# Optimization experiments

Hardware: AMD Instinct MI355X
Metric: run time of the kernel (lower is better)

## Reference

```python
import jax, jax.numpy as jnp
import numpy as np

N = 4096          # n_neurons
M = 10            # max_memory
T = 10            # max_ticks
B = 1024          # batch
P = N // 2 // 2   # n_pairs = 1024
AD = 64           # attention_dim


def ln(x, g, b, eps=1e-5):
    m = x.mean(-1, keepdims=True)
    v = ((x - m) ** 2).mean(-1, keepdims=True)
    return (x - m) * jax.lax.rsqrt(v + eps) * g + b


def setup_inputs() -> dict:
    key = jax.random.key(0)
    ks = iter(jax.random.split(key, 64))

    def rn(shape, s=0.05):
        return (jax.random.normal(next(ks), shape) * s).astype(jnp.float32)

    d = {}
    d['x'] = jax.random.normal(next(ks), (B, 1, 28, 28), dtype=jnp.float32)
    d['post0'] = jax.random.normal(next(ks), (N, M), dtype=jnp.float32)
    d['pre0'] = jax.random.normal(next(ks), (N, M), dtype=jnp.float32)
    d['pairs'] = jax.random.randint(next(ks), (P, 2), 0, N)
    d['decay'] = jnp.full((P,), 0.1, jnp.float32)
    # image encoder: 784 -> 128 -> 32 -> 4
    d['ie_w1'] = rn((784, 128)); d['ie_b1'] = jnp.zeros(128); d['ie_g1'] = jnp.ones(128); d['ie_be1'] = jnp.zeros(128)
    d['ie_w2'] = rn((128, 32));  d['ie_b2'] = jnp.zeros(32);  d['ie_g2'] = jnp.ones(32);  d['ie_be2'] = jnp.zeros(32)
    d['ie_w3'] = rn((32, 4));    d['ie_b3'] = jnp.zeros(4)
    # synapse model: (4+N) -> 256 -> N
    d['sy_w1'] = rn((4 + N, 256)); d['sy_b1'] = jnp.zeros(256); d['sy_g'] = jnp.ones(256); d['sy_be'] = jnp.zeros(256)
    d['sy_w2'] = rn((256, N));     d['sy_b2'] = jnp.zeros(N)
    # batched per-neuron models: M -> 128 -> 1
    d['nm_w1'] = rn((N, M, 128)); d['nm_b1'] = jnp.zeros((N, 128))
    d['nm_g'] = jnp.ones((N, 128)); d['nm_be'] = jnp.zeros((N, 128))
    d['nm_w2'] = rn((N, 128));    d['nm_b2'] = jnp.zeros(N)
    # attention projections
    d['key_w'] = rn((4, AD)); d['key_b'] = jnp.zeros(AD)
    d['val_w'] = rn((4, AD)); d['val_b'] = jnp.zeros(AD)
    d['q_w'] = rn((P, AD));   d['q_b'] = jnp.zeros(AD)
    # syncronization reader: (AD+P) -> 512 -> 64 -> 10
    d['rd_w1'] = rn((AD + P, 512)); d['rd_b1'] = jnp.zeros(512); d['rd_g1'] = jnp.ones(512); d['rd_be1'] = jnp.zeros(512)
    d['rd_w2'] = rn((512, 64));     d['rd_b2'] = jnp.zeros(64);  d['rd_g2'] = jnp.ones(64);  d['rd_be2'] = jnp.zeros(64)
    d['rd_w3'] = rn((64, 10));      d['rd_b3'] = jnp.zeros(10)
    return d


def reference(x, post0, pre0, pairs, decay,
              ie_w1, ie_b1, ie_g1, ie_be1, ie_w2, ie_b2, ie_g2, ie_be2, ie_w3, ie_b3,
              sy_w1, sy_b1, sy_g, sy_be, sy_w2, sy_b2,
              nm_w1, nm_b1, nm_g, nm_be, nm_w2, nm_b2,
              key_w, key_b, val_w, val_b, q_w, q_b,
              rd_w1, rd_b1, rd_g1, rd_be1, rd_w2, rd_b2, rd_g2, rd_be2, rd_w3, rd_b3):
    b = x.shape[0]
    fx = x.reshape(b, -1)
    # image encoder
    e = jax.nn.relu(ln(fx @ ie_w1 + ie_b1, ie_g1, ie_be1))
    e = jax.nn.relu(ln(e @ ie_w2 + ie_b2, ie_g2, ie_be2))
    enc = e @ ie_w3 + ie_b3                               # [B,4]
    keys = enc @ key_w + key_b                            # [B,AD]
    values = enc @ val_w + val_b                          # [B,AD]
    post, pre = post0, pre0
    pred = None
    for tick in range(T):
        last_post = jnp.broadcast_to(post[:, -1][None, :], (b, N))
        syn_in = jnp.concatenate([enc, last_post], axis=1)            # [B,4+N]
        h = jax.nn.relu(ln(syn_in @ sy_w1 + sy_b1, sy_g, sy_be))
        new_pre = h @ sy_w2 + sy_b2                                   # [B,N]
        pre = jnp.concatenate([pre[:, 1:], new_pre.mean(0)[:, None]], axis=1)
        # batched per-neuron MLP over history
        h2 = jax.nn.relu(ln(jnp.einsum('nm,nmh->nh', pre, nm_w1) + nm_b1, nm_g, nm_be))
        new_post = jnp.einsum('nh,nh->n', h2, nm_w2) + nm_b2          # [N]
        post = jnp.concatenate([post[:, 1:], new_post[:, None]], axis=1)
        # decayed pair synchronization
        L = min(tick + 1, M)
        Zi = post[pairs[:, 0], M - L:]                                # [P,L]
        Zj = post[pairs[:, 1], M - L:]
        td = jnp.arange(L - 1, -1, -1, dtype=post.dtype)              # [L]
        R = jnp.exp(-decay[:, None] * td[None, :])                    # [P,L]
        sync = jnp.sum(Zi * R * Zj, axis=1) / (jnp.sum(R, axis=1) + 1e-8)  # [P]
        sv = jnp.broadcast_to(sync[None, :], (b, P))                  # [B,P]
        q = sv @ q_w + q_b                                            # [B,AD]
        scores = jnp.sum(q * keys, axis=-1, keepdims=True) / jnp.sqrt(jnp.float32(AD))
        aw = jax.nn.softmax(scores, axis=-1)                          # [B,1] -> ones
        att = aw * values                                             # [B,AD]
        comb = jnp.concatenate([att, sv], axis=-1)                    # [B,AD+P]
        r = jax.nn.relu(ln(comb @ rd_w1 + rd_b1, rd_g1, rd_be1))
        r = jax.nn.relu(ln(r @ rd_w2 + rd_b2, rd_g2, rd_be2))
        pred = r @ rd_w3 + rd_b3                                      # [B,10]
    return pred
```

## Files before the change

### kernel.cpp

```cpp
#include <hip/hip_runtime.h>

#define N_ 4096
#define M_ 10
#define T_ 10
#define B_ 1024
#define P_ 1024
#define NBLK 256
#define NTHR 512

__device__ __forceinline__ float wave_red_sum(float v) {
#pragma unroll
  for (int m = 32; m >= 1; m >>= 1) v += __shfl_xor(v, m);
  return v;
}

__device__ __forceinline__ float gld(const float* p) {
  return __hip_atomic_load(p, __ATOMIC_RELAXED, __HIP_MEMORY_SCOPE_AGENT);
}
__device__ __forceinline__ void gst(float* p, float v) {
  __hip_atomic_store(p, v, __ATOMIC_RELAXED, __HIP_MEMORY_SCOPE_AGENT);
}
__device__ __forceinline__ unsigned ld_u(unsigned* p) {
  return __hip_atomic_load(p, __ATOMIC_RELAXED, __HIP_MEMORY_SCOPE_AGENT);
}

__device__ __forceinline__ void drain_sync() {
  asm volatile("s_waitcnt vmcnt(0)" ::: "memory");
  __syncthreads();
}
__device__ __forceinline__ void arrive8(unsigned* line8, int g) {
  if (threadIdx.x == 0)
    __hip_atomic_fetch_add(&line8[(g & 7) * 32], 1u, __ATOMIC_RELAXED, __HIP_MEMORY_SCOPE_AGENT);
}
__device__ __forceinline__ void wait_sum8(unsigned* line8, unsigned target) {
  if (threadIdx.x == 0) {
    unsigned s;
    do {
      s = 0;
#pragma unroll
      for (int i = 0; i < 8; ++i) s += ld_u(&line8[i * 32]);
      if (s < target) __builtin_amdgcn_s_sleep(1);
    } while (s < target);
  }
  __syncthreads();
}
__device__ __forceinline__ void wait_word(unsigned* f, unsigned target) {
  if (threadIdx.x == 0) {
    while (ld_u(f) < target) __builtin_amdgcn_s_sleep(1);
  }
  __syncthreads();
}

__global__ void k_init(unsigned* __restrict__ bar) {
  if (threadIdx.x < 1024)
    __hip_atomic_store(bar + threadIdx.x, 0u, __ATOMIC_RELAXED, __HIP_MEMORY_SCOPE_AGENT);
}

struct MArgs {
  const float *x, *post0, *pre0;
  const int* pairs;
  const float* decay;
  const float *iew1, *ieb1, *ieg1, *iebe1, *iew2, *ieb2, *ieg2, *iebe2, *iew3, *ieb3;
  const float *syw1, *syb1, *syg, *sybe, *syw2, *syb2;
  const float *nw1, *nb1, *ng, *nbe, *nw2, *nb2;
  const float *vw, *vb;
  const float *rdw1, *rdb1, *rdg1, *rdbe1, *rdw2, *rdb2, *rdg2, *rdbe2, *rdw3, *rdb3;
  float *pc, *pc2, *enc_g, *hbar, *postG, *syncv, *scp, *cstat;
  float* out;
  unsigned* bar;
};

__global__ __launch_bounds__(NTHR)
void k_mega(MArgs a) {
  const int g = blockIdx.x, tid = threadIdx.x;
  const int lane = tid & 63;
  const int n0 = g * 16, b0e = g * 4;

  __shared__ float s_w1[16 * M_ * 128];
  __shared__ float s_syw1[16 * 256];
  __shared__ float s_w4[4 * 256];
  __shared__ float reg1[4096];
  __shared__ float reg2[1024];
  __shared__ float s_mbrb[2048];
  __shared__ float s_values[4][64];
  __shared__ float s_post[16][M_];
  __shared__ float s_pre[16][M_];
  __shared__ float s_pl[16];
  __shared__ float s_hbar[256];
  __shared__ float s_tmp[2][256];
  __shared__ float s_red[16];
  __shared__ float s_stats[20];
  __shared__ float s_static[14];

  unsigned* barA = a.bar;
  unsigned* barC = a.bar + 256;
  unsigned* barR = a.bar + 512;
  unsigned* flagB = a.bar + 544;

  {
    const float4* src = (const float4*)(a.nw1 + n0 * M_ * 128);
    float4* dst = (float4*)s_w1;
    for (int i = tid; i < 16 * M_ * 128 / 4; i += NTHR) dst[i] = src[i];
    const float4* s2 = (const float4*)(a.syw1 + (4 + n0) * 256);
    float4* d2 = (float4*)s_syw1;
    for (int i = tid; i < 16 * 256 / 4; i += NTHR) d2[i] = s2[i];
    const float4* s3 = (const float4*)a.syw1;
    float4* d3 = (float4*)s_w4;
    for (int i = tid; i < 1024 / 4; i += NTHR) d3[i] = s3[i];
    if (tid < 160) {
      int r = tid / 10, m = tid - r * 10;
      s_post[r][m] = a.post0[(n0 + r) * M_ + m];
      s_pre[r][m]  = a.pre0[(n0 + r) * M_ + m];
    }
    for (int i = tid; i < 4 * 784; i += NTHR) reg1[i] = a.x[b0e * 784 + i];
  }
  __syncthreads();
  if (tid < 16) s_pl[tid] = s_post[tid][M_ - 1];

  {
    int r = tid >> 7, j = tid & 127;
    float u = a.ieb1[j];
    const float* fxr = reg1 + r * 784;
    for (int k = 0; k < 784; ++k) u += fxr[k] * a.iew1[k * 128 + j];
    float s = wave_red_sum(u), sq = wave_red_sum(u * u);
    int w = tid >> 6;
    if (lane == 0) { s_tmp[0][w] = s; s_tmp[1][w] = sq; }
    __syncthreads();
    float S = s_tmp[0][r * 2] + s_tmp[0][r * 2 + 1];
    float S2 = s_tmp[1][r * 2] + s_tmp[1][r * 2 + 1];
    float mm = S * (1.f / 128.f), vv = S2 * (1.f / 128.f) - mm * mm;
    reg2[r * 128 + j] = fmaxf((u - mm) * rsqrtf(vv + 1e-5f) * a.ieg1[j] + a.iebe1[j], 0.f);
  }
  __syncthreads();
  if (tid < 128) {
    int r = tid >> 5, jj = tid & 31;
    float u = a.ieb2[jj];
    for (int k = 0; k < 128; ++k) u += reg2[r * 128 + k] * a.iew2[k * 32 + jj];
    float ss = u, sq = u * u;
#pragma unroll
    for (int m = 16; m >= 1; m >>= 1) { ss += __shfl_xor(ss, m, 32); sq += __shfl_xor(sq, m, 32); }
    float mm = ss * (1.f / 32.f), vv = sq * (1.f / 32.f) - mm * mm;
    reg2[512 + r * 32 + jj] = fmaxf((u - mm) * rsqrtf(vv + 1e-5f) * a.ieg2[jj] + a.iebe2[jj], 0.f);
  }
  __syncthreads();
  if (tid < 16) {
    int r = tid >> 2, o = tid & 3;
    float u = a.ieb3[o];
    for (int k = 0; k < 32; ++k) u += reg2[512 + r * 32 + k] * a.iew3[k * 4 + o];
    reg2[640 + r * 4 + o] = u;
    gst(&a.enc_g[(b0e + r) * 4 + o], u);
  }
  __syncthreads();
  if (tid < 256) {
    int r = tid >> 6, v = tid & 63;
    float u = a.vb[v];
#pragma unroll
    for (int o = 0; o < 4; ++o) u += reg2[640 + r * 4 + o] * a.vw[o * 64 + v];
    s_values[r][v] = u;
  }
  __syncthreads();
  {
    int j = tid & 255, half = tid >> 8;
    float acc = 0.f;
#pragma unroll
    for (int r = 0; r < 8; ++r) {
      int n = half * 8 + r;
      acc += s_pl[n] * s_syw1[n * 256 + j];
    }
    s_tmp[half][j] = acc;
  }
  __syncthreads();
  if (tid < 256) gst(&a.pc[g * 256 + tid], s_tmp[0][tid] + s_tmp[1][tid]);
  drain_sync();
  arrive8(barA, g);

  for (int t = 0; t < T_; ++t) {
    if (g < 8) {
      wait_sum8(barA, 256u * (unsigned)(t + 1));
      int j = tid & 255, half = tid >> 8;
      float acc = 0.f;
#pragma unroll
      for (int r = 0; r < 16; ++r)
        acc += gld(&a.pc[(g * 32 + half * 16 + r) * 256 + j]);
      s_tmp[half][j] = acc;
      __syncthreads();
      if (tid < 256) gst(&a.pc2[g * 256 + tid], s_tmp[0][tid] + s_tmp[1][tid]);
      drain_sync();
      if (tid == 0)
        __hip_atomic_fetch_add(barR, 1u, __ATOMIC_RELAXED, __HIP_MEMORY_SCOPE_AGENT);
    }
    if (g == 0) {
      wait_word(barR, 8u * (unsigned)(t + 1));
      float cv = 0.f;
      if (tid < 256) {
        cv = a.syb1[tid];
#pragma unroll
        for (int s = 0; s < 8; ++s) cv += gld(&a.pc2[s * 256 + tid]);
      }
      if (t == 0) {
        float q[14];
        if (tid < 256) {
          float wv[4] = {s_w4[tid], s_w4[256 + tid], s_w4[512 + tid], s_w4[768 + tid]};
          int idx = 0;
#pragma unroll
          for (int o = 0; o < 4; ++o) q[idx++] = wv[o];
#pragma unroll
          for (int o = 0; o < 4; ++o)
#pragma unroll
            for (int p = 0; p <= o; ++p) q[idx++] = wv[o] * wv[p];
        } else {
#pragma unroll
          for (int i = 0; i < 14; ++i) q[i] = 0.f;
        }
#pragma unroll
        for (int i = 0; i < 14; ++i) q[i] = wave_red_sum(q[i]);
        int w = tid >> 6;
        if (lane == 0) {
#pragma unroll
          for (int i = 0; i < 14; ++i) s_tmp[1][w * 16 + i] = q[i];
        }
        __syncthreads();
        if (tid < 14) {
          float S = 0.f;
#pragma unroll
          for (int w2 = 0; w2 < 8; ++w2) S += s_tmp[1][w2 * 16 + tid];
          s_static[tid] = S * (1.f / 256.f);
        }
        __syncthreads();
      }
      {
        float p[6];
        if (tid < 256) {
          p[0] = cv; p[1] = cv * cv;
          p[2] = cv * s_w4[tid]; p[3] = cv * s_w4[256 + tid];
          p[4] = cv * s_w4[512 + tid]; p[5] = cv * s_w4[768 + tid];
        } else {
#pragma unroll
          for (int i = 0; i < 6; ++i) p[i] = 0.f;
        }
#pragma unroll
        for (int i = 0; i < 6; ++i) p[i] = wave_red_sum(p[i]);
        int w = tid >> 6;
        if (lane == 0) {
#pragma unroll
          for (int i = 0; i < 6; ++i) s_tmp[0][w * 8 + i] = p[i];
        }
        __syncthreads();
        if (tid < 6) {
          float S = 0.f;
#pragma unroll
          for (int w2 = 0; w2 < 8; ++w2) S += s_tmp[0][w2 * 8 + tid];
          gst(&a.cstat[256 + tid], S * (1.f / 256.f));
        }
      }
      if (tid < 256) gst(&a.cstat[tid], cv);
      if (tid < 14) gst(&a.cstat[262 + tid], s_static[tid]);
      drain_sync();
      if (tid == 0)
        __hip_atomic_store(flagB, (unsigned)(t + 1), __ATOMIC_RELAXED, __HIP_MEMORY_SCOPE_AGENT);
    }
    if (g < 64) {
      wait_word(flagB, (unsigned)(t + 1));
      if (t == 0) {
        for (int i = tid; i < 4096; i += NTHR) {
          int b = i >> 2, o = i & 3;
          reg1[o * 1024 + b] = gld(&a.enc_g[i]);
        }
      }
      if (tid < 20) s_stats[tid] = gld(&a.cstat[256 + tid]);
      if (tid < 4)  s_red[tid] = gld(&a.cstat[4 * g + tid]);
      __syncthreads();
      for (int b = tid; b < 1024; b += NTHR) {
        float e0 = reg1[b], e1v = reg1[1024 + b], e2v = reg1[2048 + b], e3v = reg1[3072 + b];
        float m = s_stats[0] + e0 * s_stats[6] + e1v * s_stats[7] + e2v * s_stats[8] + e3v * s_stats[9];
        float eu2 = s_stats[1] + 2.f * (e0 * s_stats[2] + e1v * s_stats[3] + e2v * s_stats[4] + e3v * s_stats[5]);
        float qf = e0 * e0 * s_stats[10]
                 + 2.f * e1v * e0 * s_stats[11] + e1v * e1v * s_stats[12]
                 + 2.f * e2v * e0 * s_stats[13] + 2.f * e2v * e1v * s_stats[14] + e2v * e2v * s_stats[15]
                 + 2.f * e3v * e0 * s_stats[16] + 2.f * e3v * e1v * s_stats[17]
                 + 2.f * e3v * e2v * s_stats[18] + e3v * e3v * s_stats[19];
        eu2 += qf;
        s_mbrb[b] = m;
        s_mbrb[1024 + b] = rsqrtf(eu2 - m * m + 1e-5f);
      }
      __syncthreads();
      {
        int q = tid >> 7, bt = tid & 127;
        int jj = 4 * g + q;
        float cj = s_red[q];
        float w0 = s_w4[jj], w1v = s_w4[256 + jj], w2v = s_w4[512 + jj], w3v = s_w4[768 + jj];
        float gj = a.syg[jj], bj = a.sybe[jj];
        float acc = 0.f;
#pragma unroll
        for (int bb = 0; bb < 8; ++bb) {
          int b = bb * 128 + bt;
          float u = cj + reg1[b] * w0 + reg1[1024 + b] * w1v + reg1[2048 + b] * w2v + reg1[3072 + b] * w3v;
          float y = (u - s_mbrb[b]) * s_mbrb[1024 + b] * gj + bj;
          acc += fmaxf(y, 0.f);
        }
        acc = wave_red_sum(acc);
        int wv = tid >> 6;
        if (lane == 0) s_tmp[0][wv] = acc;
        __syncthreads();
        if ((tid & 127) == 0)
          gst(&a.hbar[jj], (s_tmp[0][wv] + s_tmp[0][wv + 1]) * (1.f / 1024.f));
      }
      drain_sync();
      arrive8(barC, g);
    }
    wait_sum8(barC, 64u * (unsigned)(t + 1));
    if (tid < 256) s_hbar[tid] = gld(&a.hbar[tid]);
    __syncthreads();
    {
      int nl = tid & 15, kq = tid >> 4;
      float u = 0.f;
#pragma unroll
      for (int kk = 0; kk < 8; ++kk) {
        int k = kq * 8 + kk;
        u += s_hbar[k] * a.syw2[k * N_ + n0 + nl];
      }
      ((float*)s_tmp)[kq * 16 + nl] = u;
    }
    __syncthreads();
    if (tid < 16) {
      float v = a.syb2[n0 + tid];
#pragma unroll
      for (int q2 = 0; q2 < 32; ++q2) v += ((float*)s_tmp)[q2 * 16 + tid];
#pragma unroll
      for (int m = 0; m < M_ - 1; ++m) s_pre[tid][m] = s_pre[tid][m + 1];
      s_pre[tid][M_ - 1] = v;
    }
    __syncthreads();
    {
      int nl = tid >> 5, q = tid & 31;
      int n2 = n0 + nl;
      float pr[M_];
#pragma unroll
      for (int m = 0; m < M_; ++m) pr[m] = s_pre[nl][m];
      float u[4];
#pragma unroll
      for (int k = 0; k < 4; ++k) {
        int j = q + 32 * k;
        float uu = a.nb1[n2 * 128 + j];
#pragma unroll
        for (int m = 0; m < M_; ++m) uu += pr[m] * s_w1[(nl * M_ + m) * 128 + j];
        u[k] = uu;
      }
      float s = u[0] + u[1] + u[2] + u[3];
      float sq = u[0] * u[0] + u[1] * u[1] + u[2] * u[2] + u[3] * u[3];
#pragma unroll
      for (int m = 16; m >= 1; m >>= 1) { s += __shfl_xor(s, m, 32); sq += __shfl_xor(sq, m, 32); }
      float mm = s * (1.f / 128.f), vv = sq * (1.f / 128.f) - mm * mm;
      float ri = rsqrtf(vv + 1e-5f);
      float d = 0.f;
#pragma unroll
      for (int k = 0; k < 4; ++k) {
        int j = q + 32 * k;
        float y = fmaxf((u[k] - mm) * ri * a.ng[n2 * 128 + j] + a.nbe[n2 * 128 + j], 0.f);
        d += y * a.nw2[n2 * 128 + j];
      }
#pragma unroll
      for (int m = 16; m >= 1; m >>= 1) d += __shfl_xor(d, m, 32);
      if (q == 0) {
        float npost = d + a.nb2[n2];
#pragma unroll
        for (int m = 0; m < M_ - 1; ++m) s_post[nl][m] = s_post[nl][m + 1];
        s_post[nl][M_ - 1] = npost;
        s_pl[nl] = npost;
      }
    }
    __syncthreads();
    if (t < T_ - 1) {
      int j = tid & 255, half = tid >> 8;
      float acc = 0.f;
#pragma unroll
      for (int r = 0; r < 8; ++r) {
        int n = half * 8 + r;
        acc += s_pl[n] * s_syw1[n * 256 + j];
      }
      s_tmp[half][j] = acc;
      __syncthreads();
      if (tid < 256) gst(&a.pc[g * 256 + tid], s_tmp[0][tid] + s_tmp[1][tid]);
    } else {
      if (tid < 160) {
        int r = tid / 10, m = tid - r * 10;
        gst(&a.postG[(n0 + r) * M_ + m], s_post[r][m]);
      }
    }
    drain_sync();
    arrive8(barA, g);
  }

  wait_sum8(barA, 256u * 11u);
  if (tid < 4) {
    int p = g * 4 + tid;
    int i = a.pairs[p * 2], jn = a.pairs[p * 2 + 1];
    float dc = a.decay[p];
    float num = 0.f, den = 0.f;
#pragma unroll
    for (int l = 0; l < M_; ++l) {
      float r = expf(-dc * (float)(M_ - 1 - l));
      num += gld(&a.postG[i * M_ + l]) * r * gld(&a.postG[jn * M_ + l]);
      den += r;
    }
    gst(&a.syncv[p], num / (den + 1e-8f));
  }
  drain_sync();
  arrive8(barA, g);
  if (g < 8) {
    wait_sum8(barA, 256u * 12u);
    if (tid < 128) s_tmp[0][tid] = gld(&a.syncv[g * 128 + tid]);
    __syncthreads();
    float acc = 0.f;
    for (int i = 0; i < 128; ++i)
      acc += s_tmp[0][i] * a.rdw1[(64 + g * 128 + i) * 512 + tid];
    gst(&a.scp[g * 512 + tid], acc);
    drain_sync();
    arrive8(barC, g);
  }
  wait_sum8(barC, 64u * 10u + 8u);
  {
    float* r1 = reg1;
    float* p2 = reg1 + 2048;
    float base = a.rdb1[tid];
#pragma unroll
    for (int s = 0; s < 8; ++s) base += gld(&a.scp[s * 512 + tid]);
    float u[4];
#pragma unroll
    for (int r = 0; r < 4; ++r) u[r] = base;
    for (int k = 0; k < 64; ++k) {
      float w = a.rdw1[k * 512 + tid];
#pragma unroll
      for (int r = 0; r < 4; ++r) u[r] += s_values[r][k] * w;
    }
    int wid = tid >> 6;
#pragma unroll
    for (int r = 0; r < 4; ++r) {
      float s = wave_red_sum(u[r]), sq = wave_red_sum(u[r] * u[r]);
      if (lane == 0) { s_tmp[0][r * 8 + wid] = s; s_tmp[1][r * 8 + wid] = sq; }
    }
    __syncthreads();
    float gg = a.rdg1[tid], bb = a.rdbe1[tid];
#pragma unroll
    for (int r = 0; r < 4; ++r) {
      float S = 0.f, S2 = 0.f;
#pragma unroll
      for (int w = 0; w < 8; ++w) { S += s_tmp[0][r * 8 + w]; S2 += s_tmp[1][r * 8 + w]; }
      float m = S * (1.f / 512.f), v = S2 * (1.f / 512.f) - m * m;
      r1[r * 512 + tid] = fmaxf((u[r] - m) * rsqrtf(v + 1e-5f) * gg + bb, 0.f);
    }
    __syncthreads();
    int o = tid & 63, kq = tid >> 6;
    float u2[4] = {0.f, 0.f, 0.f, 0.f};
#pragma unroll
    for (int kk = 0; kk < 64; ++kk) {
      int k = kq * 64 + kk;
      float w = a.rdw2[k * 64 + o];
#pragma unroll
      for (int r = 0; r < 4; ++r) u2[r] += r1[r * 512 + k] * w;
    }
#pragma unroll
    for (int r = 0; r < 4; ++r) p2[(kq * 4 + r) * 64 + o] = u2[r];
    __syncthreads();
    if (tid < 256) {
      int r = tid >> 6, o2 = tid & 63;
      float v = a.rdb2[o2];
#pragma unroll
      for (int q = 0; q < 8; ++q) v += p2[(q * 4 + r) * 64 + o2];
      float s = wave_red_sum(v), sq = wave_red_sum(v * v);
      float m = s * (1.f / 64.f), var = sq * (1.f / 64.f) - m * m;
      reg2[r * 64 + o2] = fmaxf((v - m) * rsqrtf(var + 1e-5f) * a.rdg2[o2] + a.rdbe2[o2], 0.f);
    }
    __syncthreads();
    if (tid < 40) {
      int r = tid / 10, o3 = tid - r * 10;
      float acc = a.rdb3[o3];
#pragma unroll
      for (int k = 0; k < 64; ++k) acc += reg2[r * 64 + k] * a.rdw3[k * 10 + o3];
      a.out[(b0e + r) * 10 + o3] = acc;
    }
  }
}

extern "C" void kernel_launch(void* const* d_in, const int* in_sizes, int n_in,
                              void* d_out, int out_size, void* d_ws, size_t ws_size,
                              hipStream_t stream) {
  MArgs a;
  a.x     = (const float*)d_in[0];
  a.post0 = (const float*)d_in[1];
  a.pre0  = (const float*)d_in[2];
  a.pairs = (const int*)d_in[3];
  a.decay = (const float*)d_in[4];
  a.iew1  = (const float*)d_in[5];
  a.ieb1  = (const float*)d_in[6];
  a.ieg1  = (const float*)d_in[7];
  a.iebe1 = (const float*)d_in[8];
  a.iew2  = (const float*)d_in[9];
  a.ieb2  = (const float*)d_in[10];
  a.ieg2  = (const float*)d_in[11];
  a.iebe2 = (const float*)d_in[12];
  a.iew3  = (const float*)d_in[13];
  a.ieb3  = (const float*)d_in[14];
  a.syw1  = (const float*)d_in[15];
  a.syb1  = (const float*)d_in[16];
  a.syg   = (const float*)d_in[17];
  a.sybe  = (const float*)d_in[18];
  a.syw2  = (const float*)d_in[19];
  a.syb2  = (const float*)d_in[20];
  a.nw1   = (const float*)d_in[21];
  a.nb1   = (const float*)d_in[22];
  a.ng    = (const float*)d_in[23];
  a.nbe   = (const float*)d_in[24];
  a.nw2   = (const float*)d_in[25];
  a.nb2   = (const float*)d_in[26];
  a.vw    = (const float*)d_in[29];
  a.vb    = (const float*)d_in[30];
  a.rdw1  = (const float*)d_in[33];
  a.rdb1  = (const float*)d_in[34];
  a.rdg1  = (const float*)d_in[35];
  a.rdbe1 = (const float*)d_in[36];
  a.rdw2  = (const float*)d_in[37];
  a.rdb2  = (const float*)d_in[38];
  a.rdg2  = (const float*)d_in[39];
  a.rdbe2 = (const float*)d_in[40];
  a.rdw3  = (const float*)d_in[41];
  a.rdb3  = (const float*)d_in[42];
  a.out = (float*)d_out;

  float* ws = (float*)d_ws;
  a.pc    = ws;
  a.pc2   = ws + 65536;
  a.enc_g = ws + 67584;
  a.hbar  = ws + 71680;
  a.postG = ws + 71936;
  a.syncv = ws + 112896;
  a.scp   = ws + 113920;
  a.cstat = ws + 118016;
  a.bar   = (unsigned*)(ws + 118528);

  k_init<<<1, 1024, 0, stream>>>(a.bar);
  k_mega<<<NBLK, NTHR, 0, stream>>>(a);
}
```

Baseline: 198.0 us.

## Replace counter barriers with per-block flag slots and redundantly compute stats

Swaps atomic-add counter barriers for per-block monotonic flag slots that waiting blocks poll in parallel across a wavefront. The serial block-0 stage that computed hidden-layer stats and republished them is removed: every block now sums the partials and computes the stats itself. The hidden-unit work is spread over all 256 blocks, one unit each, instead of 64 blocks. The pair-sync pass is folded into the 8 reader blocks, which drops one grid-wide barrier. This removes several serialized grid barrier hops per tick, in exchange for redundant reductions and more polling traffic.

```diff
diff --git a/kernel.cpp b/kernel.cpp
--- a/kernel.cpp
+++ b/kernel.cpp
@@ -28,25 +28,32 @@
   asm volatile("s_waitcnt vmcnt(0)" ::: "memory");
   __syncthreads();
 }
-__device__ __forceinline__ void arrive8(unsigned* line8, int g) {
+__device__ __forceinline__ void signal(unsigned* slot, unsigned val) {
   if (threadIdx.x == 0)
-    __hip_atomic_fetch_add(&line8[(g & 7) * 32], 1u, __ATOMIC_RELAXED, __HIP_MEMORY_SCOPE_AGENT);
-}
-__device__ __forceinline__ void wait_sum8(unsigned* line8, unsigned target) {
-  if (threadIdx.x == 0) {
-    unsigned s;
+    __hip_atomic_store(slot, val, __ATOMIC_RELAXED, __HIP_MEMORY_SCOPE_AGENT);
+}
+__device__ __forceinline__ void wait_set(unsigned* slots, int n, unsigned target) {
+  if (threadIdx.x < 64) {
+    int lane = threadIdx.x;
+    bool ok;
     do {
-      s = 0;
-#pragma unroll
-      for (int i = 0; i < 8; ++i) s += ld_u(&line8[i * 32]);
-      if (s < target) __builtin_amdgcn_s_sleep(1);
-    } while (s < target);
-  }
-  __syncthreads();
-}
-__device__ __forceinline__ void wait_word(unsigned* f, unsigned target) {
-  if (threadIdx.x == 0) {
-    while (ld_u(f) < target) __builtin_amdgcn_s_sleep(1);
+      ok = true;
+      for (int i = lane; i < n; i += 64) ok &= (ld_u(&slots[i]) >= target);
+      ok = __all(ok);
+      if (!ok) __builtin_amdgcn_s_sleep(1);
+    } while (!ok);
+  }
+  __syncthreads();
+}
+__device__ __forceinline__ void wait_mod8(unsigned* slots, int s, unsigned target) {
+  if (threadIdx.x < 64) {
+    int lane = threadIdx.x;
+    bool ok;
+    do {
+      ok = (lane < 32) ? (ld_u(&slots[s + 8 * lane]) >= target) : true;
+      ok = __all(ok);
+      if (!ok) __builtin_amdgcn_s_sleep(1);
+    } while (!ok);
   }
   __syncthreads();
 }
@@ -65,7 +72,7 @@
   const float *nw1, *nb1, *ng, *nbe, *nw2, *nb2;
   const float *vw, *vb;
   const float *rdw1, *rdb1, *rdg1, *rdbe1, *rdw2, *rdb2, *rdg2, *rdbe2, *rdw3, *rdb3;
-  float *pc, *pc2, *enc_g, *hbar, *postG, *syncv, *scp, *cstat;
+  float *pc, *pc2, *enc_g, *hbar, *postG, *scp;
   float* out;
   unsigned* bar;
 };
@@ -87,15 +94,13 @@
   __shared__ float s_pre[16][M_];
   __shared__ float s_pl[16];
   __shared__ float s_hbar[256];
+  __shared__ float s_cval[256];
   __shared__ float s_tmp[2][256];
-  __shared__ float s_red[16];
   __shared__ float s_stats[20];
-  __shared__ float s_static[14];
-
-  unsigned* barA = a.bar;
-  unsigned* barC = a.bar + 256;
-  unsigned* barR = a.bar + 512;
-  unsigned* flagB = a.bar + 544;
+
+  unsigned* slotA = a.bar;
+  unsigned* slotR = a.bar + 256;
+  unsigned* slotC = a.bar + 320;
 
   {
     const float4* src = (const float4*)(a.nw1 + n0 * M_ * 128);
@@ -172,105 +177,100 @@
   __syncthreads();
   if (tid < 256) gst(&a.pc[g * 256 + tid], s_tmp[0][tid] + s_tmp[1][tid]);
   drain_sync();
-  arrive8(barA, g);
+  signal(&slotA[g], 1u);
+
+  {
+    float q[14];
+    if (tid < 256) {
+      float wv[4] = {s_w4[tid], s_w4[256 + tid], s_w4[512 + tid], s_w4[768 + tid]};
+      int idx = 0;
+#pragma unroll
+      for (int o = 0; o < 4; ++o) q[idx++] = wv[o];
+#pragma unroll
+      for (int o = 0; o < 4; ++o)
+#pragma unroll
+        for (int p = 0; p <= o; ++p) q[idx++] = wv[o] * wv[p];
+    } else {
+#pragma unroll
+      for (int i = 0; i < 14; ++i) q[i] = 0.f;
+    }
+#pragma unroll
+    for (int i = 0; i < 14; ++i) q[i] = wave_red_sum(q[i]);
+    int w = tid >> 6;
+    if (lane == 0) {
+#pragma unroll
+      for (int i = 0; i < 14; ++i) s_tmp[1][w * 16 + i] = q[i];
+    }
+    __syncthreads();
+    if (tid < 14) {
+      float S = 0.f;
+#pragma unroll
+      for (int w2 = 0; w2 < 8; ++w2) S += s_tmp[1][w2 * 16 + tid];
+      s_stats[6 + tid] = S * (1.f / 256.f);
+    }
+  }
+  __syncthreads();
 
   for (int t = 0; t < T_; ++t) {
     if (g < 8) {
-      wait_sum8(barA, 256u * (unsigned)(t + 1));
+      wait_mod8(slotA, g, (unsigned)(t + 1));
       int j = tid & 255, half = tid >> 8;
       float acc = 0.f;
 #pragma unroll
-      for (int r = 0; r < 16; ++r)
-        acc += gld(&a.pc[(g * 32 + half * 16 + r) * 256 + j]);
+      for (int i = 0; i < 16; ++i) {
+        int r = g + 8 * (half * 16 + i);
+        acc += gld(&a.pc[r * 256 + j]);
+      }
       s_tmp[half][j] = acc;
       __syncthreads();
       if (tid < 256) gst(&a.pc2[g * 256 + tid], s_tmp[0][tid] + s_tmp[1][tid]);
       drain_sync();
-      if (tid == 0)
-        __hip_atomic_fetch_add(barR, 1u, __ATOMIC_RELAXED, __HIP_MEMORY_SCOPE_AGENT);
-    }
-    if (g == 0) {
-      wait_word(barR, 8u * (unsigned)(t + 1));
+      signal(&slotR[g], (unsigned)(t + 1));
+    }
+    wait_set(slotR, 8, (unsigned)(t + 1));
+    if (t == 0) {
+      for (int i = tid; i < 4096; i += NTHR) {
+        int b = i >> 2, o = i & 3;
+        reg1[o * 1024 + b] = gld(&a.enc_g[i]);
+      }
+    }
+    {
       float cv = 0.f;
       if (tid < 256) {
         cv = a.syb1[tid];
 #pragma unroll
         for (int s = 0; s < 8; ++s) cv += gld(&a.pc2[s * 256 + tid]);
-      }
-      if (t == 0) {
-        float q[14];
-        if (tid < 256) {
-          float wv[4] = {s_w4[tid], s_w4[256 + tid], s_w4[512 + tid], s_w4[768 + tid]};
-          int idx = 0;
-#pragma unroll
-          for (int o = 0; o < 4; ++o) q[idx++] = wv[o];
-#pragma unroll
-          for (int o = 0; o < 4; ++o)
-#pragma unroll
-            for (int p = 0; p <= o; ++p) q[idx++] = wv[o] * wv[p];
-        } else {
-#pragma unroll
-          for (int i = 0; i < 14; ++i) q[i] = 0.f;
-        }
-#pragma unroll
-        for (int i = 0; i < 14; ++i) q[i] = wave_red_sum(q[i]);
-        int w = tid >> 6;
-        if (lane == 0) {
-#pragma unroll
-          for (int i = 0; i < 14; ++i) s_tmp[1][w * 16 + i] = q[i];
-        }
-        __syncthreads();
-        if (tid < 14) {
-          float S = 0.f;
-#pragma unroll
-          for (int w2 = 0; w2 < 8; ++w2) S += s_tmp[1][w2 * 16 + tid];
-          s_static[tid] = S * (1.f / 256.f);
-        }
-        __syncthreads();
-      }
-      {
-        float p[6];
-        if (tid < 256) {
-          p[0] = cv; p[1] = cv * cv;
-          p[2] = cv * s_w4[tid]; p[3] = cv * s_w4[256 + tid];
-          p[4] = cv * s_w4[512 + tid]; p[5] = cv * s_w4[768 + tid];
-        } else {
-#pragma unroll
-          for (int i = 0; i < 6; ++i) p[i] = 0.f;
-        }
-#pragma unroll
-        for (int i = 0; i < 6; ++i) p[i] = wave_red_sum(p[i]);
-        int w = tid >> 6;
-        if (lane == 0) {
-#pragma unroll
-          for (int i = 0; i < 6; ++i) s_tmp[0][w * 8 + i] = p[i];
-        }
-        __syncthreads();
-        if (tid < 6) {
-          float S = 0.f;
-#pragma unroll
-          for (int w2 = 0; w2 < 8; ++w2) S += s_tmp[0][w2 * 8 + tid];
-          gst(&a.cstat[256 + tid], S * (1.f / 256.f));
-        }
-      }
-      if (tid < 256) gst(&a.cstat[tid], cv);
-      if (tid < 14) gst(&a.cstat[262 + tid], s_static[tid]);
-      drain_sync();
-      if (tid == 0)
-        __hip_atomic_store(flagB, (unsigned)(t + 1), __ATOMIC_RELAXED, __HIP_MEMORY_SCOPE_AGENT);
-    }
-    if (g < 64) {
-      wait_word(flagB, (unsigned)(t + 1));
-      if (t == 0) {
-        for (int i = tid; i < 4096; i += NTHR) {
-          int b = i >> 2, o = i & 3;
-          reg1[o * 1024 + b] = gld(&a.enc_g[i]);
-        }
-      }
-      if (tid < 20) s_stats[tid] = gld(&a.cstat[256 + tid]);
-      if (tid < 4)  s_red[tid] = gld(&a.cstat[4 * g + tid]);
+        s_cval[tid] = cv;
+      }
+      float p[6];
+      if (tid < 256) {
+        p[0] = cv; p[1] = cv * cv;
+        p[2] = cv * s_w4[tid]; p[3] = cv * s_w4[256 + tid];
+        p[4] = cv * s_w4[512 + tid]; p[5] = cv * s_w4[768 + tid];
+      } else {
+#pragma unroll
+        for (int i = 0; i < 6; ++i) p[i] = 0.f;
+      }
+#pragma unroll
+      for (int i = 0; i < 6; ++i) p[i] = wave_red_sum(p[i]);
+      int w = tid >> 6;
+      if (lane == 0) {
+#pragma unroll
+        for (int i = 0; i < 6; ++i) s_tmp[0][w * 8 + i] = p[i];
+      }
       __syncthreads();
-      for (int b = tid; b < 1024; b += NTHR) {
+      if (tid < 6) {
+        float S = 0.f;
+#pragma unroll
+        for (int w2 = 0; w2 < 8; ++w2) S += s_tmp[0][w2 * 8 + tid];
+        s_stats[tid] = S * (1.f / 256.f);
+      }
+      __syncthreads();
+    }
+    {
+#pragma unroll
+      for (int h2 = 0; h2 < 2; ++h2) {
+        int b = h2 * 512 + tid;
         float e0 = reg1[b], e1v = reg1[1024 + b], e2v = reg1[2048 + b], e3v = reg1[3072 + b];
         float m = s_stats[0] + e0 * s_stats[6] + e1v * s_stats[7] + e2v * s_stats[8] + e3v * s_stats[9];
         float eu2 = s_stats[1] + 2.f * (e0 * s_stats[2] + e1v * s_stats[3] + e2v * s_stats[4] + e3v * s_stats[5]);
@@ -284,31 +284,33 @@
         s_mbrb[1024 + b] = rsqrtf(eu2 - m * m + 1e-5f);
       }
       __syncthreads();
-      {
-        int q = tid >> 7, bt = tid & 127;
-        int jj = 4 * g + q;
-        float cj = s_red[q];
-        float w0 = s_w4[jj], w1v = s_w4[256 + jj], w2v = s_w4[512 + jj], w3v = s_w4[768 + jj];
-        float gj = a.syg[jj], bj = a.sybe[jj];
-        float acc = 0.f;
-#pragma unroll
-        for (int bb = 0; bb < 8; ++bb) {
-          int b = bb * 128 + bt;
-          float u = cj + reg1[b] * w0 + reg1[1024 + b] * w1v + reg1[2048 + b] * w2v + reg1[3072 + b] * w3v;
-          float y = (u - s_mbrb[b]) * s_mbrb[1024 + b] * gj + bj;
-          acc += fmaxf(y, 0.f);
-        }
-        acc = wave_red_sum(acc);
-        int wv = tid >> 6;
-        if (lane == 0) s_tmp[0][wv] = acc;
-        __syncthreads();
-        if ((tid & 127) == 0)
-          gst(&a.hbar[jj], (s_tmp[0][wv] + s_tmp[0][wv + 1]) * (1.f / 1024.f));
-      }
-      drain_sync();
-      arrive8(barC, g);
-    }
-    wait_sum8(barC, 64u * (unsigned)(t + 1));
+    }
+    {
+      float cj = s_cval[g];
+      float w0 = s_w4[g], w1v = s_w4[256 + g], w2v = s_w4[512 + g], w3v = s_w4[768 + g];
+      float gj = a.syg[g], bj = a.sybe[g];
+      float acc = 0.f;
+#pragma unroll
+      for (int h2 = 0; h2 < 2; ++h2) {
+        int b = h2 * 512 + tid;
+        float u = cj + reg1[b] * w0 + reg1[1024 + b] * w1v + reg1[2048 + b] * w2v + reg1[3072 + b] * w3v;
+        float y = (u - s_mbrb[b]) * s_mbrb[1024 + b] * gj + bj;
+        acc += fmaxf(y, 0.f);
+      }
+      acc = wave_red_sum(acc);
+      int w = tid >> 6;
+      if (lane == 0) s_tmp[0][w] = acc;
+      __syncthreads();
+      if (tid == 0) {
+        float S = 0.f;
+#pragma unroll
+        for (int w2 = 0; w2 < 8; ++w2) S += s_tmp[0][w2];
+        gst(&a.hbar[g], S * (1.f / 1024.f));
+      }
+    }
+    drain_sync();
+    signal(&slotC[g], (unsigned)(t + 1));
+    wait_set(slotC, 256, (unsigned)(t + 1));
     if (tid < 256) s_hbar[tid] = gld(&a.hbar[tid]);
     __syncthreads();
     {
@@ -388,37 +390,33 @@
       }
     }
     drain_sync();
-    arrive8(barA, g);
-  }
-
-  wait_sum8(barA, 256u * 11u);
-  if (tid < 4) {
-    int p = g * 4 + tid;
-    int i = a.pairs[p * 2], jn = a.pairs[p * 2 + 1];
-    float dc = a.decay[p];
-    float num = 0.f, den = 0.f;
-#pragma unroll
-    for (int l = 0; l < M_; ++l) {
-      float r = expf(-dc * (float)(M_ - 1 - l));
-      num += gld(&a.postG[i * M_ + l]) * r * gld(&a.postG[jn * M_ + l]);
-      den += r;
-    }
-    gst(&a.syncv[p], num / (den + 1e-8f));
-  }
-  drain_sync();
-  arrive8(barA, g);
+    signal(&slotA[g], (unsigned)(t + 2));
+  }
+
   if (g < 8) {
-    wait_sum8(barA, 256u * 12u);
-    if (tid < 128) s_tmp[0][tid] = gld(&a.syncv[g * 128 + tid]);
+    wait_set(slotA, 256, 11u);
+    if (tid < 128) {
+      int p = g * 128 + tid;
+      int i = a.pairs[p * 2], jn = a.pairs[p * 2 + 1];
+      float dc = a.decay[p];
+      float num = 0.f, den = 0.f;
+#pragma unroll
+      for (int l = 0; l < M_; ++l) {
+        float r = expf(-dc * (float)(M_ - 1 - l));
+        num += gld(&a.postG[i * M_ + l]) * r * gld(&a.postG[jn * M_ + l]);
+        den += r;
+      }
+      s_tmp[0][tid] = num / (den + 1e-8f);
+    }
     __syncthreads();
     float acc = 0.f;
     for (int i = 0; i < 128; ++i)
       acc += s_tmp[0][i] * a.rdw1[(64 + g * 128 + i) * 512 + tid];
     gst(&a.scp[g * 512 + tid], acc);
     drain_sync();
-    arrive8(barC, g);
-  }
-  wait_sum8(barC, 64u * 10u + 8u);
+    signal(&slotR[g], 11u);
+  }
+  wait_set(slotR, 8, 11u);
   {
     float* r1 = reg1;
     float* p2 = reg1 + 2048;
@@ -533,10 +531,8 @@
   a.enc_g = ws + 67584;
   a.hbar  = ws + 71680;
   a.postG = ws + 71936;
-  a.syncv = ws + 112896;
-  a.scp   = ws + 113920;
-  a.cstat = ws + 118016;
-  a.bar   = (unsigned*)(ws + 118528);
+  a.scp   = ws + 112896;
+  a.bar   = (unsigned*)(ws + 117000);
 
   k_init<<<1, 1024, 0, stream>>>(a.bar);
   k_mega<<<NBLK, NTHR, 0, stream>>>(a);
```

After: 194.2 us. Within noise of the previous version (-1.9%).
